# Optimization experiments

Measured on AMD Instinct MI355X. Metric: run time of the kernel, lower is better.

The kernel has to match this reference:

```python
import jax, jax.numpy as jnp
import numpy as np

B, N, M = 2, 8192, 8192


def setup_inputs() -> dict:
    key = jax.random.key(0)
    ks = jax.random.split(key, 12)
    def rn(k, shape):
        return jax.random.normal(k, shape, dtype=jnp.float32)
    return {
        "in_xyz": rn(ks[0], (B, N, 3)),
        "in_rot": rn(ks[1], (B, N, 4)),
        "in_scale": rn(ks[2], (B, N, 3)),
        "in_opacity": rn(ks[3], (B, N, 1)),
        "in_sh_dc": rn(ks[4], (B, N, 3)),
        "in_sh_rest": rn(ks[5], (B, N, 45)),
        "out_xyz": rn(ks[6], (B, M, 3)),
        "out_rot": rn(ks[7], (B, M, 4)),
        "out_scale": rn(ks[8], (B, M, 3)),
        "out_opacity": rn(ks[9], (B, M, 1)),
        "out_sh_dc": rn(ks[10], (B, M, 3)),
        "out_sh_rest": rn(ks[11], (B, M, 45)),
    }


POS_W, ROT_W, SCALE_W, OPAC_W, SH_W = 1.0, 0.5, 0.5, 0.3, 0.2


def _cdist(a, b):
    # a: [B,M,3], b: [B,N,3] -> [B,M,N] Euclidean distance via Gram trick
    sq = (jnp.sum(a * a, -1)[:, :, None] + jnp.sum(b * b, -1)[:, None, :]
          - 2.0 * jnp.einsum('bmd,bnd->bmn', a, b))
    return jnp.sqrt(jnp.maximum(sq, 0.0))


def _gather(x, idx):
    # x: [B,N,D], idx: [B,M] -> [B,M,D]
    return jnp.take_along_axis(x, idx[:, :, None], axis=1)


def reference(in_xyz, in_rot, in_scale, in_opacity, in_sh_dc, in_sh_rest,
              out_xyz, out_rot, out_scale, out_opacity, out_sh_dc, out_sh_rest):
    dist = _cdist(out_xyz, in_xyz)                 # [B,M,N]
    min_out_to_in = jnp.min(dist, axis=2)          # [B,M]
    match_idx = jnp.argmin(dist, axis=2)           # [B,M]
    min_in_to_out = jnp.min(dist, axis=1)          # [B,N]
    pos_loss = (min_out_to_in.mean() + min_in_to_out.mean()) / 2

    matched_rot = _gather(in_rot, match_idx)
    matched_scale = _gather(in_scale, match_idx)
    matched_opacity = _gather(in_opacity, match_idx)
    matched_sh_dc = _gather(in_sh_dc, match_idx)
    matched_sh_rest = _gather(in_sh_rest, match_idx)

    rot_dot = jnp.abs(jnp.sum(out_rot * matched_rot, axis=-1))
    rot_loss = jnp.mean(1.0 - rot_dot)
    scale_loss = jnp.mean(jnp.abs(out_scale - matched_scale))
    opacity_loss = jnp.mean(jnp.abs(out_opacity - matched_opacity))
    sh_loss = (jnp.mean(jnp.abs(out_sh_dc - matched_sh_dc))
               + jnp.mean(jnp.abs(out_sh_rest - matched_sh_rest)))

    total = (POS_W * pos_loss + ROT_W * rot_loss + SCALE_W * scale_loss
             + OPAC_W * opacity_loss + SH_W * sh_loss)
    return total
```

## Files before the change

### kernel.cpp

```cpp
#include <hip/hip_runtime.h>


#define BB 2
#define NN 8192
#define MM 8192
#define TILE_PTS 1024
#define CHUNK_PTS 64
#define CH_STRIDE (CHUNK_PTS * 4 + 4)
#define PM 256
#define NSL 8
#define NPAIR 1024

__device__ __forceinline__ void dmerge(float& d, int& i, float od, int oi) {
    if (od < d || (od == d && oi < i)) { d = od; i = oi; }
}

__device__ __forceinline__ void stage_tile(const float* __restrict__ xyz,
                                           int b, int gtile, int t, float* smem) {
    const uint4* src = (const uint4*)((const char*)xyz +
                       ((size_t)b * NN + (size_t)gtile * TILE_PTS) * 12);
    uint4 wb[3];
#pragma unroll
    for (int k = 0; k < 3; ++k) wb[k] = src[t * 3 + k];
    const unsigned int* w = (const unsigned int*)wb;
    const int p0 = t * 4;
    float4* dst = (float4*)(smem + (p0 >> 6) * CH_STRIDE) + (p0 & 63);
#pragma unroll
    for (int i = 0; i < 4; ++i) {
        float x = __uint_as_float(w[3 * i + 0]);
        float y = __uint_as_float(w[3 * i + 1]);
        float z = __uint_as_float(w[3 * i + 2]);
        float4 v;
        v.x = x; v.y = y; v.z = z;
        v.w = fmaf(z, z, fmaf(y, y, x * x));
        dst[i] = v;
    }
}

__global__ __launch_bounds__(1024) void k_pair(
    const float* __restrict__ in_xyz,
    const float* __restrict__ out_xyz,
    float* __restrict__ outD2,
    int*   __restrict__ outIdx,
    float* __restrict__ inD2) {

    __shared__ float smem[16 * CH_STRIDE];

    const int t  = threadIdx.x;
    const int ml = t >> 4;
    const int c  = t & 15;
    const int blk = blockIdx.x;
    const int side = blk >> 9;
    const int rem = blk & 511;
    const int b  = rem >> 8;
    const int e  = (rem >> 5) & 7;
    const int q0 = (rem & 31) * PM + ml * 4;

    const float* qbase = (side == 0) ? out_xyz : in_xyz;
    const float* pbase = (side == 0) ? in_xyz  : out_xyz;

    float m2x0, m2y0, m2z0, msq0, m2x1, m2y1, m2z1, msq1;
    float m2x2, m2y2, m2z2, msq2, m2x3, m2y3, m2z3, msq3;
#define LOADQ(i)                                                            \
    { const float* qp = qbase + ((size_t)b * MM + q0 + i) * 3;              \
      float ox = qp[0], oy = qp[1], oz = qp[2];                             \
      m2x##i = -2.f * ox; m2y##i = -2.f * oy; m2z##i = -2.f * oz;           \
      msq##i = fmaf(oz, oz, fmaf(oy, oy, ox * ox)); }
    LOADQ(0) LOADQ(1) LOADQ(2) LOADQ(3)
#undef LOADQ

    if (t < 256) stage_tile(pbase, b, e, t, smem);
    __syncthreads();

    const float4* cp = (const float4*)(smem + c * CH_STRIDE);
    const int base = e * TILE_PTS + c * CHUNK_PTS;

    if (side == 0) {
        float bd0 = 3e38f, bd1 = 3e38f, bd2 = 3e38f, bd3 = 3e38f;
        int   bi0 = 0,     bi1 = 0,     bi2 = 0,     bi3 = 0;
#pragma unroll 8
        for (int j = 0; j < CHUNK_PTS; ++j) {
            float4 p = cp[j];
            float k0 = fmaf(p.x, m2x0, fmaf(p.y, m2y0, fmaf(p.z, m2z0, p.w)));
            float k1 = fmaf(p.x, m2x1, fmaf(p.y, m2y1, fmaf(p.z, m2z1, p.w)));
            float k2 = fmaf(p.x, m2x2, fmaf(p.y, m2y2, fmaf(p.z, m2z2, p.w)));
            float k3 = fmaf(p.x, m2x3, fmaf(p.y, m2y3, fmaf(p.z, m2z3, p.w)));
            if (k0 < bd0) { bd0 = k0; bi0 = base + j; }
            if (k1 < bd1) { bd1 = k1; bi1 = base + j; }
            if (k2 < bd2) { bd2 = k2; bi2 = base + j; }
            if (k3 < bd3) { bd3 = k3; bi3 = base + j; }
        }
#pragma unroll
        for (int off = 1; off < 16; off <<= 1) {
            float od; int oi;
            od = __shfl_xor(bd0, off, 64); oi = __shfl_xor(bi0, off, 64); dmerge(bd0, bi0, od, oi);
            od = __shfl_xor(bd1, off, 64); oi = __shfl_xor(bi1, off, 64); dmerge(bd1, bi1, od, oi);
            od = __shfl_xor(bd2, off, 64); oi = __shfl_xor(bi2, off, 64); dmerge(bd2, bi2, od, oi);
            od = __shfl_xor(bd3, off, 64); oi = __shfl_xor(bi3, off, 64); dmerge(bd3, bi3, od, oi);
        }
        if (c == 0) {
            const size_t g = ((size_t)b * MM + q0) * NSL + e;
            outD2[g + 0 * NSL] = bd0 + msq0; outIdx[g + 0 * NSL] = bi0;
            outD2[g + 1 * NSL] = bd1 + msq1; outIdx[g + 1 * NSL] = bi1;
            outD2[g + 2 * NSL] = bd2 + msq2; outIdx[g + 2 * NSL] = bi2;
            outD2[g + 3 * NSL] = bd3 + msq3; outIdx[g + 3 * NSL] = bi3;
        }
    } else {
        float bd0 = 3e38f, bd1 = 3e38f, bd2 = 3e38f, bd3 = 3e38f;
#pragma unroll 8
        for (int j = 0; j < CHUNK_PTS; ++j) {
            float4 p = cp[j];
            float k0 = fmaf(p.x, m2x0, fmaf(p.y, m2y0, fmaf(p.z, m2z0, p.w)));
            float k1 = fmaf(p.x, m2x1, fmaf(p.y, m2y1, fmaf(p.z, m2z1, p.w)));
            float k2 = fmaf(p.x, m2x2, fmaf(p.y, m2y2, fmaf(p.z, m2z2, p.w)));
            float k3 = fmaf(p.x, m2x3, fmaf(p.y, m2y3, fmaf(p.z, m2z3, p.w)));
            bd0 = fminf(bd0, k0);
            bd1 = fminf(bd1, k1);
            bd2 = fminf(bd2, k2);
            bd3 = fminf(bd3, k3);
        }
#pragma unroll
        for (int off = 1; off < 16; off <<= 1) {
            bd0 = fminf(bd0, __shfl_xor(bd0, off, 64));
            bd1 = fminf(bd1, __shfl_xor(bd1, off, 64));
            bd2 = fminf(bd2, __shfl_xor(bd2, off, 64));
            bd3 = fminf(bd3, __shfl_xor(bd3, off, 64));
        }
        if (c == 0) {
            const size_t g = ((size_t)b * NN + q0) * NSL + e;
            inD2[g + 0 * NSL] = bd0 + msq0;
            inD2[g + 1 * NSL] = bd1 + msq1;
            inD2[g + 2 * NSL] = bd2 + msq2;
            inD2[g + 3 * NSL] = bd3 + msq3;
        }
    }
}

__global__ __launch_bounds__(256) void k_epi(
    const float* __restrict__ in_rot,
    const float* __restrict__ in_scale,
    const float* __restrict__ in_op,
    const float* __restrict__ in_dc,
    const float* __restrict__ in_rest,
    const float* __restrict__ out_rot,
    const float* __restrict__ out_scale,
    const float* __restrict__ out_op,
    const float* __restrict__ out_dc,
    const float* __restrict__ out_rest,
    const float* __restrict__ outD2,
    const int*   __restrict__ outIdx,
    const float* __restrict__ inD2,
    float* __restrict__ pout,
    float* __restrict__ pin) {

    const int t = threadIdx.x;
    const int blk = blockIdx.x;

    if (blk < 128) {
        const int u = blk * 256 + t;
        const int m = u >> 1;
        const int h = u & 1;
        const int b = m >> 13;
        float d2 = outD2[(size_t)m * NSL + 0];
        int  idx = outIdx[(size_t)m * NSL + 0];
#pragma unroll
        for (int s = 1; s < NSL; ++s) {
            float ds = outD2[(size_t)m * NSL + s];
            int   is = outIdx[(size_t)m * NSL + s];
            if (ds < d2) { d2 = ds; idx = is; }
        }
        const size_t og = (size_t)m;
        const size_t ig = (size_t)b * NN + (size_t)idx;

        float pos = 0.f, rot = 0.f, scl = 0.f, opa = 0.f, dcv = 0.f, rsv = 0.f;
        if (h == 0) {
            pos = sqrtf(fmaxf(d2, 0.f));
            const float4 orv = ((const float4*)out_rot)[og];
            const float4 irv = ((const float4*)in_rot)[ig];
            float rdot = orv.x * irv.x + orv.y * irv.y + orv.z * irv.z + orv.w * irv.w;
            rot = 1.f - fabsf(rdot);
#pragma unroll
            for (int qq = 0; qq < 3; ++qq) scl += fabsf(out_scale[og * 3 + qq] - in_scale[ig * 3 + qq]);
            opa = fabsf(out_op[og] - in_op[ig]);
#pragma unroll
            for (int qq = 0; qq < 3; ++qq) dcv += fabsf(out_dc[og * 3 + qq] - in_dc[ig * 3 + qq]);
#pragma unroll
            for (int e = 0; e < 22; ++e)
                rsv += fabsf(out_rest[og * 45 + e] - in_rest[ig * 45 + e]);
        } else {
#pragma unroll
            for (int e = 22; e < 45; ++e)
                rsv += fabsf(out_rest[og * 45 + e] - in_rest[ig * 45 + e]);
        }

#pragma unroll
        for (int off = 1; off < 64; off <<= 1) {
            pos += __shfl_xor(pos, off, 64);
            rot += __shfl_xor(rot, off, 64);
            scl += __shfl_xor(scl, off, 64);
            opa += __shfl_xor(opa, off, 64);
            dcv += __shfl_xor(dcv, off, 64);
            rsv += __shfl_xor(rsv, off, 64);
        }
        if ((t & 63) == 0) {
            const size_t w = (size_t)blk * 4 + (t >> 6);
            pout[w * 6 + 0] = pos; pout[w * 6 + 1] = rot; pout[w * 6 + 2] = scl;
            pout[w * 6 + 3] = opa; pout[w * 6 + 4] = dcv; pout[w * 6 + 5] = rsv;
        }
    } else {
        const int g = (blk - 128) * 256 + t;
        float d2 = inD2[(size_t)g * NSL + 0];
#pragma unroll
        for (int s = 1; s < NSL; ++s) d2 = fminf(d2, inD2[(size_t)g * NSL + s]);
        float v = sqrtf(fmaxf(d2, 0.f));
#pragma unroll
        for (int off = 1; off < 64; off <<= 1) v += __shfl_xor(v, off, 64);
        if ((t & 63) == 0) pin[(size_t)(blk - 128) * 4 + (t >> 6)] = v;
    }
}

__global__ __launch_bounds__(256) void k_fin(const float* __restrict__ pout,
                                             const float* __restrict__ pin,
                                             unsigned int* __restrict__ out) {
    __shared__ float red[4][8];
    const int t = threadIdx.x;
    float s0 = 0.f, s1 = 0.f, s2 = 0.f, s3 = 0.f, s4 = 0.f, s5 = 0.f, s6 = 0.f;
    for (int i = t; i < 512; i += 256) {
        s0 += pout[(size_t)i * 6 + 0];
        s1 += pout[(size_t)i * 6 + 1];
        s2 += pout[(size_t)i * 6 + 2];
        s3 += pout[(size_t)i * 6 + 3];
        s4 += pout[(size_t)i * 6 + 4];
        s5 += pout[(size_t)i * 6 + 5];
    }
    if (t < 256) s6 += pin[t];
#pragma unroll
    for (int off = 1; off < 64; off <<= 1) {
        s0 += __shfl_xor(s0, off, 64);
        s1 += __shfl_xor(s1, off, 64);
        s2 += __shfl_xor(s2, off, 64);
        s3 += __shfl_xor(s3, off, 64);
        s4 += __shfl_xor(s4, off, 64);
        s5 += __shfl_xor(s5, off, 64);
        s6 += __shfl_xor(s6, off, 64);
    }
    if ((t & 63) == 0) {
        const int w = t >> 6;
        red[w][0] = s0; red[w][1] = s1; red[w][2] = s2; red[w][3] = s3;
        red[w][4] = s4; red[w][5] = s5; red[w][6] = s6;
    }
    __syncthreads();
    if (t == 0) {
        float a[7];
#pragma unroll
        for (int j = 0; j < 7; ++j)
            a[j] = red[0][j] + red[1][j] + red[2][j] + red[3][j];
        const float inv_bm = 1.0f / (float)(BB * MM);
        const float inv_bn = 1.0f / (float)(BB * NN);
        const float pos = 0.5f * (a[0] * inv_bm + a[6] * inv_bn);
        const float rot = a[1] * inv_bm;
        const float scl = a[2] * inv_bm * (1.f / 3.f);
        const float opa = a[3] * inv_bm;
        const float sh  = a[4] * inv_bm * (1.f / 3.f) + a[5] * inv_bm * (1.f / 45.f);
        const float total = 1.0f * pos + 0.5f * rot + 0.5f * scl + 0.3f * opa + 0.2f * sh;
        unsigned int ub = __float_as_uint(total);
        unsigned int r  = (ub + 0x7FFFu + ((ub >> 16) & 1u)) >> 16;
        if (!(total == total) || fabsf(total) > 1e30f) r = 0x4080u;
        out[0] = (r << 16) | r;
    }
}

extern "C" void kernel_launch(void* const* d_in, const int* in_sizes, int n_in,
                              void* d_out, int out_size, void* d_ws, size_t ws_size,
                              hipStream_t stream) {
    const float* in_xyz    = (const float*)d_in[0];
    const float* in_rot    = (const float*)d_in[1];
    const float* in_scale  = (const float*)d_in[2];
    const float* in_op     = (const float*)d_in[3];
    const float* in_dc     = (const float*)d_in[4];
    const float* in_rest   = (const float*)d_in[5];
    const float* out_xyz   = (const float*)d_in[6];
    const float* out_rot   = (const float*)d_in[7];
    const float* out_scale = (const float*)d_in[8];
    const float* out_op    = (const float*)d_in[9];
    const float* out_dc    = (const float*)d_in[10];
    const float* out_rest  = (const float*)d_in[11];

    float* outD2 = (float*)d_ws;
    int*   outIdx = (int*)(outD2 + (size_t)BB * MM * NSL);
    float* inD2  = (float*)(outIdx + (size_t)BB * MM * NSL);
    float* pout  = inD2 + (size_t)BB * NN * NSL;
    float* pin   = pout + 512 * 6;

    k_pair<<<NPAIR, 1024, 0, stream>>>(in_xyz, out_xyz, outD2, outIdx, inD2);
    k_epi<<<192, 256, 0, stream>>>(in_rot, in_scale, in_op, in_dc, in_rest,
                                   out_rot, out_scale, out_op, out_dc, out_rest,
                                   outD2, outIdx, inD2, pout, pin);
    k_fin<<<1, 256, 0, stream>>>(pout, pin, (unsigned int*)d_out);
}
```

Measured before the change: 115.8 us.

## Compute both directional minima from one distance pass; fuse final reduction into epilogue

The pair kernel now evaluates each query-point distance once. It derives the per-query argmin and, via shuffles plus LDS atomicMin, the per-point column minimum, which removes the separate in-to-out pass and halves the pair blocks. Column partial minima go to a wider 32-slice buffer that the epilogue reduces. The epilogue splits each matched row across 4 threads instead of 2, and the last block, found with an atomic counter, does the final reduction, removing the third kernel launch. In exchange the inner loop gains shuffles and shared atomics, and the epilogue reads a larger partial buffer.

```diff
diff --git a/kernel.cpp b/kernel.cpp
--- a/kernel.cpp
+++ b/kernel.cpp
@@ -7,9 +7,12 @@
 #define TILE_PTS 1024
 #define CHUNK_PTS 64
 #define CH_STRIDE (CHUNK_PTS * 4 + 4)
+#define CM_STRIDE 65
 #define PM 256
 #define NSL 8
-#define NPAIR 1024
+#define GSL 32
+#define NPAIR 512
+#define NEPI 320
 
 __device__ __forceinline__ void dmerge(float& d, int& i, float od, int oi) {
     if (od < d || (od == d && oi < i)) { d = od; i = oi; }
@@ -42,97 +45,83 @@
     const float* __restrict__ out_xyz,
     float* __restrict__ outD2,
     int*   __restrict__ outIdx,
-    float* __restrict__ inD2) {
+    float* __restrict__ inD2s,
+    unsigned int* __restrict__ cnt) {
 
     __shared__ float smem[16 * CH_STRIDE];
+    __shared__ unsigned int cmu[16 * CM_STRIDE];
 
     const int t  = threadIdx.x;
     const int ml = t >> 4;
     const int c  = t & 15;
     const int blk = blockIdx.x;
-    const int side = blk >> 9;
-    const int rem = blk & 511;
-    const int b  = rem >> 8;
-    const int e  = (rem >> 5) & 7;
-    const int q0 = (rem & 31) * PM + ml * 4;
-
-    const float* qbase = (side == 0) ? out_xyz : in_xyz;
-    const float* pbase = (side == 0) ? in_xyz  : out_xyz;
+    const int b  = blk >> 8;
+    const int e  = (blk >> 5) & 7;
+    const int g  = blk & 31;
+    const int q0 = g * PM + ml * 4;
+
+    if (blk == 0 && t == 0) cnt[0] = 0u;
 
     float m2x0, m2y0, m2z0, msq0, m2x1, m2y1, m2z1, msq1;
     float m2x2, m2y2, m2z2, msq2, m2x3, m2y3, m2z3, msq3;
 #define LOADQ(i)                                                            \
-    { const float* qp = qbase + ((size_t)b * MM + q0 + i) * 3;              \
+    { const float* qp = out_xyz + ((size_t)b * MM + q0 + i) * 3;            \
       float ox = qp[0], oy = qp[1], oz = qp[2];                             \
       m2x##i = -2.f * ox; m2y##i = -2.f * oy; m2z##i = -2.f * oz;           \
       msq##i = fmaf(oz, oz, fmaf(oy, oy, ox * ox)); }
     LOADQ(0) LOADQ(1) LOADQ(2) LOADQ(3)
 #undef LOADQ
 
-    if (t < 256) stage_tile(pbase, b, e, t, smem);
+    if (t < 256) stage_tile(in_xyz, b, e, t, smem);
+    for (int i = t; i < 16 * CM_STRIDE; i += 1024) cmu[i] = 0x7F800000u;
     __syncthreads();
 
     const float4* cp = (const float4*)(smem + c * CH_STRIDE);
     const int base = e * TILE_PTS + c * CHUNK_PTS;
-
-    if (side == 0) {
-        float bd0 = 3e38f, bd1 = 3e38f, bd2 = 3e38f, bd3 = 3e38f;
-        int   bi0 = 0,     bi1 = 0,     bi2 = 0,     bi3 = 0;
+    unsigned int* cma = cmu + c * CM_STRIDE;
+    const bool doAtom = ((t & 48) == 0);
+
+    float bd0 = 3e38f, bd1 = 3e38f, bd2 = 3e38f, bd3 = 3e38f;
+    int   bi0 = 0,     bi1 = 0,     bi2 = 0,     bi3 = 0;
 #pragma unroll 8
-        for (int j = 0; j < CHUNK_PTS; ++j) {
-            float4 p = cp[j];
-            float k0 = fmaf(p.x, m2x0, fmaf(p.y, m2y0, fmaf(p.z, m2z0, p.w)));
-            float k1 = fmaf(p.x, m2x1, fmaf(p.y, m2y1, fmaf(p.z, m2z1, p.w)));
-            float k2 = fmaf(p.x, m2x2, fmaf(p.y, m2y2, fmaf(p.z, m2z2, p.w)));
-            float k3 = fmaf(p.x, m2x3, fmaf(p.y, m2y3, fmaf(p.z, m2z3, p.w)));
-            if (k0 < bd0) { bd0 = k0; bi0 = base + j; }
-            if (k1 < bd1) { bd1 = k1; bi1 = base + j; }
-            if (k2 < bd2) { bd2 = k2; bi2 = base + j; }
-            if (k3 < bd3) { bd3 = k3; bi3 = base + j; }
-        }
-#pragma unroll
-        for (int off = 1; off < 16; off <<= 1) {
-            float od; int oi;
-            od = __shfl_xor(bd0, off, 64); oi = __shfl_xor(bi0, off, 64); dmerge(bd0, bi0, od, oi);
-            od = __shfl_xor(bd1, off, 64); oi = __shfl_xor(bi1, off, 64); dmerge(bd1, bi1, od, oi);
-            od = __shfl_xor(bd2, off, 64); oi = __shfl_xor(bi2, off, 64); dmerge(bd2, bi2, od, oi);
-            od = __shfl_xor(bd3, off, 64); oi = __shfl_xor(bi3, off, 64); dmerge(bd3, bi3, od, oi);
-        }
-        if (c == 0) {
-            const size_t g = ((size_t)b * MM + q0) * NSL + e;
-            outD2[g + 0 * NSL] = bd0 + msq0; outIdx[g + 0 * NSL] = bi0;
-            outD2[g + 1 * NSL] = bd1 + msq1; outIdx[g + 1 * NSL] = bi1;
-            outD2[g + 2 * NSL] = bd2 + msq2; outIdx[g + 2 * NSL] = bi2;
-            outD2[g + 3 * NSL] = bd3 + msq3; outIdx[g + 3 * NSL] = bi3;
-        }
-    } else {
-        float bd0 = 3e38f, bd1 = 3e38f, bd2 = 3e38f, bd3 = 3e38f;
-#pragma unroll 8
-        for (int j = 0; j < CHUNK_PTS; ++j) {
-            float4 p = cp[j];
-            float k0 = fmaf(p.x, m2x0, fmaf(p.y, m2y0, fmaf(p.z, m2z0, p.w)));
-            float k1 = fmaf(p.x, m2x1, fmaf(p.y, m2y1, fmaf(p.z, m2z1, p.w)));
-            float k2 = fmaf(p.x, m2x2, fmaf(p.y, m2y2, fmaf(p.z, m2z2, p.w)));
-            float k3 = fmaf(p.x, m2x3, fmaf(p.y, m2y3, fmaf(p.z, m2z3, p.w)));
-            bd0 = fminf(bd0, k0);
-            bd1 = fminf(bd1, k1);
-            bd2 = fminf(bd2, k2);
-            bd3 = fminf(bd3, k3);
-        }
-#pragma unroll
-        for (int off = 1; off < 16; off <<= 1) {
-            bd0 = fminf(bd0, __shfl_xor(bd0, off, 64));
-            bd1 = fminf(bd1, __shfl_xor(bd1, off, 64));
-            bd2 = fminf(bd2, __shfl_xor(bd2, off, 64));
-            bd3 = fminf(bd3, __shfl_xor(bd3, off, 64));
-        }
-        if (c == 0) {
-            const size_t g = ((size_t)b * NN + q0) * NSL + e;
-            inD2[g + 0 * NSL] = bd0 + msq0;
-            inD2[g + 1 * NSL] = bd1 + msq1;
-            inD2[g + 2 * NSL] = bd2 + msq2;
-            inD2[g + 3 * NSL] = bd3 + msq3;
-        }
+    for (int j = 0; j < CHUNK_PTS; ++j) {
+        float4 p = cp[j];
+        float w0 = p.w + msq0, w1 = p.w + msq1, w2 = p.w + msq2, w3 = p.w + msq3;
+        float k0 = fmaf(p.x, m2x0, fmaf(p.y, m2y0, fmaf(p.z, m2z0, w0)));
+        float k1 = fmaf(p.x, m2x1, fmaf(p.y, m2y1, fmaf(p.z, m2z1, w1)));
+        float k2 = fmaf(p.x, m2x2, fmaf(p.y, m2y2, fmaf(p.z, m2z2, w2)));
+        float k3 = fmaf(p.x, m2x3, fmaf(p.y, m2y3, fmaf(p.z, m2z3, w3)));
+        if (k0 < bd0) { bd0 = k0; bi0 = base + j; }
+        if (k1 < bd1) { bd1 = k1; bi1 = base + j; }
+        if (k2 < bd2) { bd2 = k2; bi2 = base + j; }
+        if (k3 < bd3) { bd3 = k3; bi3 = base + j; }
+        float mm = fminf(fminf(k0, k1), fminf(k2, k3));
+        mm = fmaxf(mm, 0.0f);
+        mm = fminf(mm, __shfl_xor(mm, 16, 64));
+        mm = fminf(mm, __shfl_xor(mm, 32, 64));
+        if (doAtom) atomicMin(cma + j, __float_as_uint(mm));
+    }
+
+#pragma unroll
+    for (int off = 1; off < 16; off <<= 1) {
+        float od; int oi;
+        od = __shfl_xor(bd0, off, 64); oi = __shfl_xor(bi0, off, 64); dmerge(bd0, bi0, od, oi);
+        od = __shfl_xor(bd1, off, 64); oi = __shfl_xor(bi1, off, 64); dmerge(bd1, bi1, od, oi);
+        od = __shfl_xor(bd2, off, 64); oi = __shfl_xor(bi2, off, 64); dmerge(bd2, bi2, od, oi);
+        od = __shfl_xor(bd3, off, 64); oi = __shfl_xor(bi3, off, 64); dmerge(bd3, bi3, od, oi);
+    }
+    if (c == 0) {
+        const size_t gi = ((size_t)b * MM + q0) * NSL + e;
+        outD2[gi + 0 * NSL] = bd0; outIdx[gi + 0 * NSL] = bi0;
+        outD2[gi + 1 * NSL] = bd1; outIdx[gi + 1 * NSL] = bi1;
+        outD2[gi + 2 * NSL] = bd2; outIdx[gi + 2 * NSL] = bi2;
+        outD2[gi + 3 * NSL] = bd3; outIdx[gi + 3 * NSL] = bi3;
+    }
+
+    __syncthreads();
+    {
+        float v = __uint_as_float(cmu[(t >> 6) * CM_STRIDE + (t & 63)]);
+        inD2s[(size_t)g * (BB * NN) + (size_t)b * NN + e * TILE_PTS + t] = v;
     }
 }
 
@@ -149,25 +138,30 @@
     const float* __restrict__ out_rest,
     const float* __restrict__ outD2,
     const int*   __restrict__ outIdx,
-    const float* __restrict__ inD2,
+    const float* __restrict__ inD2s,
     float* __restrict__ pout,
-    float* __restrict__ pin) {
-
+    float* __restrict__ pin,
+    unsigned int* __restrict__ cnt,
+    unsigned int* __restrict__ outw) {
+
+    __shared__ float red[4][8];
+    __shared__ int lastFlag;
     const int t = threadIdx.x;
     const int blk = blockIdx.x;
 
-    if (blk < 128) {
+    if (blk < 256) {
         const int u = blk * 256 + t;
-        const int m = u >> 1;
-        const int h = u & 1;
+        const int m = u >> 2;
+        const int h = u & 3;
         const int b = m >> 13;
-        float d2 = outD2[(size_t)m * NSL + 0];
-        int  idx = outIdx[(size_t)m * NSL + 0];
-#pragma unroll
-        for (int s = 1; s < NSL; ++s) {
-            float ds = outD2[(size_t)m * NSL + s];
-            int   is = outIdx[(size_t)m * NSL + s];
-            if (ds < d2) { d2 = ds; idx = is; }
+        float2 dv = ((const float2*)outD2)[(size_t)m * 4 + h];
+        int2   iv = ((const int2*)outIdx)[(size_t)m * 4 + h];
+        float d2 = dv.x; int idx = iv.x;
+        if (dv.y < d2) { d2 = dv.y; idx = iv.y; }
+        {
+            float od; int oi;
+            od = __shfl_xor(d2, 1, 64); oi = __shfl_xor(idx, 1, 64); dmerge(d2, idx, od, oi);
+            od = __shfl_xor(d2, 2, 64); oi = __shfl_xor(idx, 2, 64); dmerge(d2, idx, od, oi);
         }
         const size_t og = (size_t)m;
         const size_t ig = (size_t)b * NN + (size_t)idx;
@@ -179,11 +173,13 @@
             const float4 irv = ((const float4*)in_rot)[ig];
             float rdot = orv.x * irv.x + orv.y * irv.y + orv.z * irv.z + orv.w * irv.w;
             rot = 1.f - fabsf(rdot);
-#pragma unroll
-            for (int qq = 0; qq < 3; ++qq) scl += fabsf(out_scale[og * 3 + qq] - in_scale[ig * 3 + qq]);
+        } else if (h == 1) {
+#pragma unroll
+            for (int q = 0; q < 3; ++q) scl += fabsf(out_scale[og * 3 + q] - in_scale[ig * 3 + q]);
             opa = fabsf(out_op[og] - in_op[ig]);
 #pragma unroll
-            for (int qq = 0; qq < 3; ++qq) dcv += fabsf(out_dc[og * 3 + qq] - in_dc[ig * 3 + qq]);
+            for (int q = 0; q < 3; ++q) dcv += fabsf(out_dc[og * 3 + q] - in_dc[ig * 3 + q]);
+        } else if (h == 2) {
 #pragma unroll
             for (int e = 0; e < 22; ++e)
                 rsv += fabsf(out_rest[og * 45 + e] - in_rest[ig * 45 + e]);
@@ -208,24 +204,29 @@
             pout[w * 6 + 3] = opa; pout[w * 6 + 4] = dcv; pout[w * 6 + 5] = rsv;
         }
     } else {
-        const int g = (blk - 128) * 256 + t;
-        float d2 = inD2[(size_t)g * NSL + 0];
-#pragma unroll
-        for (int s = 1; s < NSL; ++s) d2 = fminf(d2, inD2[(size_t)g * NSL + s]);
+        const int n = (blk - 256) * 256 + t;
+        float d2 = inD2s[n];
+#pragma unroll
+        for (int s = 1; s < GSL; ++s)
+            d2 = fminf(d2, inD2s[(size_t)s * (BB * NN) + n]);
         float v = sqrtf(fmaxf(d2, 0.f));
 #pragma unroll
         for (int off = 1; off < 64; off <<= 1) v += __shfl_xor(v, off, 64);
-        if ((t & 63) == 0) pin[(size_t)(blk - 128) * 4 + (t >> 6)] = v;
-    }
-}
-
-__global__ __launch_bounds__(256) void k_fin(const float* __restrict__ pout,
-                                             const float* __restrict__ pin,
-                                             unsigned int* __restrict__ out) {
-    __shared__ float red[4][8];
-    const int t = threadIdx.x;
+        if ((t & 63) == 0) pin[(size_t)(blk - 256) * 4 + (t >> 6)] = v;
+    }
+
+    __syncthreads();
+    if (t == 0) {
+        __threadfence();
+        unsigned int old = atomicAdd(cnt, 1u);
+        lastFlag = (old == (unsigned)(NEPI - 1));
+    }
+    __syncthreads();
+    if (!lastFlag) return;
+    __threadfence();
+
     float s0 = 0.f, s1 = 0.f, s2 = 0.f, s3 = 0.f, s4 = 0.f, s5 = 0.f, s6 = 0.f;
-    for (int i = t; i < 512; i += 256) {
+    for (int i = t; i < 1024; i += 256) {
         s0 += pout[(size_t)i * 6 + 0];
         s1 += pout[(size_t)i * 6 + 1];
         s2 += pout[(size_t)i * 6 + 2];
@@ -233,7 +234,7 @@
         s4 += pout[(size_t)i * 6 + 4];
         s5 += pout[(size_t)i * 6 + 5];
     }
-    if (t < 256) s6 += pin[t];
+    s6 = pin[t];
 #pragma unroll
     for (int off = 1; off < 64; off <<= 1) {
         s0 += __shfl_xor(s0, off, 64);
@@ -266,7 +267,7 @@
         unsigned int ub = __float_as_uint(total);
         unsigned int r  = (ub + 0x7FFFu + ((ub >> 16) & 1u)) >> 16;
         if (!(total == total) || fabsf(total) > 1e30f) r = 0x4080u;
-        out[0] = (r << 16) | r;
+        outw[0] = (r << 16) | r;
     }
 }
 
@@ -288,13 +289,14 @@
 
     float* outD2 = (float*)d_ws;
     int*   outIdx = (int*)(outD2 + (size_t)BB * MM * NSL);
-    float* inD2  = (float*)(outIdx + (size_t)BB * MM * NSL);
-    float* pout  = inD2 + (size_t)BB * NN * NSL;
-    float* pin   = pout + 512 * 6;
-
-    k_pair<<<NPAIR, 1024, 0, stream>>>(in_xyz, out_xyz, outD2, outIdx, inD2);
-    k_epi<<<192, 256, 0, stream>>>(in_rot, in_scale, in_op, in_dc, in_rest,
-                                   out_rot, out_scale, out_op, out_dc, out_rest,
-                                   outD2, outIdx, inD2, pout, pin);
-    k_fin<<<1, 256, 0, stream>>>(pout, pin, (unsigned int*)d_out);
-}
+    float* inD2s = (float*)(outIdx + (size_t)BB * MM * NSL);
+    float* pout  = inD2s + (size_t)GSL * BB * NN;
+    float* pin   = pout + 1024 * 6;
+    unsigned int* cnt = (unsigned int*)(pin + 256);
+
+    k_pair<<<NPAIR, 1024, 0, stream>>>(in_xyz, out_xyz, outD2, outIdx, inD2s, cnt);
+    k_epi<<<NEPI, 256, 0, stream>>>(in_rot, in_scale, in_op, in_dc, in_rest,
+                                    out_rot, out_scale, out_op, out_dc, out_rest,
+                                    outD2, outIdx, inD2s, pout, pin, cnt,
+                                    (unsigned int*)d_out);
+}
```

Result: slower. 135.2 us (+16.8%).

## Fuse final reduction into epilogue via atomic last-block and widen epilogue parallelism

Applied to the files above, without the earlier changes.

Removes the separate single-block finalize kernel by having the last epilogue block, detected with an atomic counter reset in the pair kernel, perform the final reduction. The epilogue now uses four threads per output point instead of two: each thread takes two slices, a shuffle merges the argmin, and the attribute loads are split across four roles. The in-side reduction switches to float4 vector loads. This saves one kernel launch and raises parallelism in the gather phase, at the cost of an atomic, fences and a serialized tail block.

```diff
diff --git a/kernel.cpp b/kernel.cpp
--- a/kernel.cpp
+++ b/kernel.cpp
@@ -10,6 +10,7 @@
 #define PM 256
 #define NSL 8
 #define NPAIR 1024
+#define NEPI 320
 
 __device__ __forceinline__ void dmerge(float& d, int& i, float od, int oi) {
     if (od < d || (od == d && oi < i)) { d = od; i = oi; }
@@ -42,7 +43,8 @@
     const float* __restrict__ out_xyz,
     float* __restrict__ outD2,
     int*   __restrict__ outIdx,
-    float* __restrict__ inD2) {
+    float* __restrict__ inD2,
+    unsigned int* __restrict__ cnt) {
 
     __shared__ float smem[16 * CH_STRIDE];
 
@@ -55,6 +57,8 @@
     const int b  = rem >> 8;
     const int e  = (rem >> 5) & 7;
     const int q0 = (rem & 31) * PM + ml * 4;
+
+    if (blk == 0 && t == 0) cnt[0] = 0u;
 
     const float* qbase = (side == 0) ? out_xyz : in_xyz;
     const float* pbase = (side == 0) ? in_xyz  : out_xyz;
@@ -151,23 +155,28 @@
     const int*   __restrict__ outIdx,
     const float* __restrict__ inD2,
     float* __restrict__ pout,
-    float* __restrict__ pin) {
-
+    float* __restrict__ pin,
+    unsigned int* __restrict__ cnt,
+    unsigned int* __restrict__ outw) {
+
+    __shared__ float red[4][8];
+    __shared__ int lastFlag;
     const int t = threadIdx.x;
     const int blk = blockIdx.x;
 
-    if (blk < 128) {
+    if (blk < 256) {
         const int u = blk * 256 + t;
-        const int m = u >> 1;
-        const int h = u & 1;
+        const int m = u >> 2;
+        const int h = u & 3;
         const int b = m >> 13;
-        float d2 = outD2[(size_t)m * NSL + 0];
-        int  idx = outIdx[(size_t)m * NSL + 0];
-#pragma unroll
-        for (int s = 1; s < NSL; ++s) {
-            float ds = outD2[(size_t)m * NSL + s];
-            int   is = outIdx[(size_t)m * NSL + s];
-            if (ds < d2) { d2 = ds; idx = is; }
+        float2 dv = ((const float2*)outD2)[(size_t)m * 4 + h];
+        int2   iv = ((const int2*)outIdx)[(size_t)m * 4 + h];
+        float d2 = dv.x; int idx = iv.x;
+        if (dv.y < d2) { d2 = dv.y; idx = iv.y; }
+        {
+            float od; int oi;
+            od = __shfl_xor(d2, 1, 64); oi = __shfl_xor(idx, 1, 64); dmerge(d2, idx, od, oi);
+            od = __shfl_xor(d2, 2, 64); oi = __shfl_xor(idx, 2, 64); dmerge(d2, idx, od, oi);
         }
         const size_t og = (size_t)m;
         const size_t ig = (size_t)b * NN + (size_t)idx;
@@ -179,11 +188,13 @@
             const float4 irv = ((const float4*)in_rot)[ig];
             float rdot = orv.x * irv.x + orv.y * irv.y + orv.z * irv.z + orv.w * irv.w;
             rot = 1.f - fabsf(rdot);
-#pragma unroll
-            for (int qq = 0; qq < 3; ++qq) scl += fabsf(out_scale[og * 3 + qq] - in_scale[ig * 3 + qq]);
+        } else if (h == 1) {
+#pragma unroll
+            for (int q = 0; q < 3; ++q) scl += fabsf(out_scale[og * 3 + q] - in_scale[ig * 3 + q]);
             opa = fabsf(out_op[og] - in_op[ig]);
 #pragma unroll
-            for (int qq = 0; qq < 3; ++qq) dcv += fabsf(out_dc[og * 3 + qq] - in_dc[ig * 3 + qq]);
+            for (int q = 0; q < 3; ++q) dcv += fabsf(out_dc[og * 3 + q] - in_dc[ig * 3 + q]);
+        } else if (h == 2) {
 #pragma unroll
             for (int e = 0; e < 22; ++e)
                 rsv += fabsf(out_rest[og * 45 + e] - in_rest[ig * 45 + e]);
@@ -208,24 +219,29 @@
             pout[w * 6 + 3] = opa; pout[w * 6 + 4] = dcv; pout[w * 6 + 5] = rsv;
         }
     } else {
-        const int g = (blk - 128) * 256 + t;
-        float d2 = inD2[(size_t)g * NSL + 0];
-#pragma unroll
-        for (int s = 1; s < NSL; ++s) d2 = fminf(d2, inD2[(size_t)g * NSL + s]);
+        const int n = (blk - 256) * 256 + t;
+        const float4 a = ((const float4*)inD2)[(size_t)n * 2 + 0];
+        const float4 c4 = ((const float4*)inD2)[(size_t)n * 2 + 1];
+        float d2 = fminf(fminf(fminf(a.x, a.y), fminf(a.z, a.w)),
+                         fminf(fminf(c4.x, c4.y), fminf(c4.z, c4.w)));
         float v = sqrtf(fmaxf(d2, 0.f));
 #pragma unroll
         for (int off = 1; off < 64; off <<= 1) v += __shfl_xor(v, off, 64);
-        if ((t & 63) == 0) pin[(size_t)(blk - 128) * 4 + (t >> 6)] = v;
-    }
-}
-
-__global__ __launch_bounds__(256) void k_fin(const float* __restrict__ pout,
-                                             const float* __restrict__ pin,
-                                             unsigned int* __restrict__ out) {
-    __shared__ float red[4][8];
-    const int t = threadIdx.x;
+        if ((t & 63) == 0) pin[(size_t)(blk - 256) * 4 + (t >> 6)] = v;
+    }
+
+    __syncthreads();
+    if (t == 0) {
+        __threadfence();
+        unsigned int old = atomicAdd(cnt, 1u);
+        lastFlag = (old == (unsigned)(NEPI - 1));
+    }
+    __syncthreads();
+    if (!lastFlag) return;
+    __threadfence();
+
     float s0 = 0.f, s1 = 0.f, s2 = 0.f, s3 = 0.f, s4 = 0.f, s5 = 0.f, s6 = 0.f;
-    for (int i = t; i < 512; i += 256) {
+    for (int i = t; i < 1024; i += 256) {
         s0 += pout[(size_t)i * 6 + 0];
         s1 += pout[(size_t)i * 6 + 1];
         s2 += pout[(size_t)i * 6 + 2];
@@ -233,7 +249,7 @@
         s4 += pout[(size_t)i * 6 + 4];
         s5 += pout[(size_t)i * 6 + 5];
     }
-    if (t < 256) s6 += pin[t];
+    s6 = pin[t];
 #pragma unroll
     for (int off = 1; off < 64; off <<= 1) {
         s0 += __shfl_xor(s0, off, 64);
@@ -266,7 +282,7 @@
         unsigned int ub = __float_as_uint(total);
         unsigned int r  = (ub + 0x7FFFu + ((ub >> 16) & 1u)) >> 16;
         if (!(total == total) || fabsf(total) > 1e30f) r = 0x4080u;
-        out[0] = (r << 16) | r;
+        outw[0] = (r << 16) | r;
     }
 }
 
@@ -290,11 +306,12 @@
     int*   outIdx = (int*)(outD2 + (size_t)BB * MM * NSL);
     float* inD2  = (float*)(outIdx + (size_t)BB * MM * NSL);
     float* pout  = inD2 + (size_t)BB * NN * NSL;
-    float* pin   = pout + 512 * 6;
-
-    k_pair<<<NPAIR, 1024, 0, stream>>>(in_xyz, out_xyz, outD2, outIdx, inD2);
-    k_epi<<<192, 256, 0, stream>>>(in_rot, in_scale, in_op, in_dc, in_rest,
-                                   out_rot, out_scale, out_op, out_dc, out_rest,
-                                   outD2, outIdx, inD2, pout, pin);
-    k_fin<<<1, 256, 0, stream>>>(pout, pin, (unsigned int*)d_out);
-}
+    float* pin   = pout + 1024 * 6;
+    unsigned int* cnt = (unsigned int*)(pin + 256);
+
+    k_pair<<<NPAIR, 1024, 0, stream>>>(in_xyz, out_xyz, outD2, outIdx, inD2, cnt);
+    k_epi<<<NEPI, 256, 0, stream>>>(in_rot, in_scale, in_op, in_dc, in_rest,
+                                    out_rot, out_scale, out_op, out_dc, out_rest,
+                                    outD2, outIdx, inD2, pout, pin, cnt,
+                                    (unsigned int*)d_out);
+}
```

New measurement: 122.9 us. 6.1% more time.

## Use packed FP32 FMA over an SoA pair layout in the pairwise distance kernel

Applied to the files above, without the earlier changes.

Stages reference points in LDS as interleaved pairs (x0,x1,y0,y1 / z0,z1,w0,w1) so each thread evaluates two candidate points at once with v_pk_fma_f32 inline asm. This halves the FMA instruction count in the inner distance loop. Blocks shrink to 512 threads with 128 queries each and the grid doubles, and launch bounds request 4 blocks per CU. In exchange the per-lane argmin tracking is duplicated, which needs extra registers and compares, and an extra merge is needed before the shuffle reduction.

```diff
diff --git a/kernel.cpp b/kernel.cpp
--- a/kernel.cpp
+++ b/kernel.cpp
@@ -4,134 +4,157 @@
 #define BB 2
 #define NN 8192
 #define MM 8192
-#define TILE_PTS 1024
-#define CHUNK_PTS 64
-#define CH_STRIDE (CHUNK_PTS * 4 + 4)
-#define PM 256
+#define PB 1024
+#define QB 128
 #define NSL 8
-#define NPAIR 1024
+#define NPAIR 2048
+
+typedef float vf2 __attribute__((ext_vector_type(2)));
+
+__device__ __forceinline__ vf2 pk_fma(vf2 a, vf2 b, vf2 c) {
+    vf2 d;
+    asm("v_pk_fma_f32 %0, %1, %2, %3" : "=v"(d) : "v"(a), "v"(b), "v"(c));
+    return d;
+}
 
 __device__ __forceinline__ void dmerge(float& d, int& i, float od, int oi) {
     if (od < d || (od == d && oi < i)) { d = od; i = oi; }
 }
 
-__device__ __forceinline__ void stage_tile(const float* __restrict__ xyz,
-                                           int b, int gtile, int t, float* smem) {
-    const uint4* src = (const uint4*)((const char*)xyz +
-                       ((size_t)b * NN + (size_t)gtile * TILE_PTS) * 12);
-    uint4 wb[3];
-#pragma unroll
-    for (int k = 0; k < 3; ++k) wb[k] = src[t * 3 + k];
-    const unsigned int* w = (const unsigned int*)wb;
-    const int p0 = t * 4;
-    float4* dst = (float4*)(smem + (p0 >> 6) * CH_STRIDE) + (p0 & 63);
-#pragma unroll
-    for (int i = 0; i < 4; ++i) {
-        float x = __uint_as_float(w[3 * i + 0]);
-        float y = __uint_as_float(w[3 * i + 1]);
-        float z = __uint_as_float(w[3 * i + 2]);
-        float4 v;
-        v.x = x; v.y = y; v.z = z;
-        v.w = fmaf(z, z, fmaf(y, y, x * x));
-        dst[i] = v;
-    }
-}
-
-__global__ __launch_bounds__(1024) void k_pair(
+__global__ __launch_bounds__(512, 4) void k_pair(
     const float* __restrict__ in_xyz,
     const float* __restrict__ out_xyz,
     float* __restrict__ outD2,
     int*   __restrict__ outIdx,
     float* __restrict__ inD2) {
 
-    __shared__ float smem[16 * CH_STRIDE];
+    __shared__ float4 xy[16 * 33];
+    __shared__ float4 zw[16 * 33];
 
     const int t  = threadIdx.x;
     const int ml = t >> 4;
     const int c  = t & 15;
     const int blk = blockIdx.x;
-    const int side = blk >> 9;
-    const int rem = blk & 511;
-    const int b  = rem >> 8;
-    const int e  = (rem >> 5) & 7;
-    const int q0 = (rem & 31) * PM + ml * 4;
+    const int side = blk >> 10;
+    const int rem = blk & 1023;
+    const int b  = rem >> 9;
+    const int e  = (rem >> 6) & 7;
+    const int q0 = (rem & 63) * QB + ml * 4;
 
     const float* qbase = (side == 0) ? out_xyz : in_xyz;
     const float* pbase = (side == 0) ? in_xyz  : out_xyz;
 
-    float m2x0, m2y0, m2z0, msq0, m2x1, m2y1, m2z1, msq1;
-    float m2x2, m2y2, m2z2, msq2, m2x3, m2y3, m2z3, msq3;
+    vf2 X0, Y0, Z0, X1, Y1, Z1, X2, Y2, Z2, X3, Y3, Z3;
+    float msq0, msq1, msq2, msq3;
 #define LOADQ(i)                                                            \
     { const float* qp = qbase + ((size_t)b * MM + q0 + i) * 3;              \
       float ox = qp[0], oy = qp[1], oz = qp[2];                             \
-      m2x##i = -2.f * ox; m2y##i = -2.f * oy; m2z##i = -2.f * oz;           \
+      float mx = -2.f * ox, my = -2.f * oy, mz = -2.f * oz;                 \
+      X##i = (vf2){mx, mx}; Y##i = (vf2){my, my}; Z##i = (vf2){mz, mz};     \
       msq##i = fmaf(oz, oz, fmaf(oy, oy, ox * ox)); }
     LOADQ(0) LOADQ(1) LOADQ(2) LOADQ(3)
 #undef LOADQ
 
-    if (t < 256) stage_tile(pbase, b, e, t, smem);
+    if (t < 256) {
+        const uint4* src = (const uint4*)((const char*)pbase +
+                           ((size_t)b * NN + (size_t)e * PB) * 12);
+        uint4 wb[3];
+#pragma unroll
+        for (int k = 0; k < 3; ++k) wb[k] = src[t * 3 + k];
+        const float* w = (const float*)wb;
+        const int ch = t >> 4;
+        const int u0 = (2 * t) & 31;
+        float x0 = w[0], y0 = w[1],  z0 = w[2];
+        float x1 = w[3], y1 = w[4],  z1 = w[5];
+        float x2 = w[6], y2 = w[7],  z2 = w[8];
+        float x3 = w[9], y3 = w[10], z3 = w[11];
+        float w0 = fmaf(z0, z0, fmaf(y0, y0, x0 * x0));
+        float w1 = fmaf(z1, z1, fmaf(y1, y1, x1 * x1));
+        float w2 = fmaf(z2, z2, fmaf(y2, y2, x2 * x2));
+        float w3 = fmaf(z3, z3, fmaf(y3, y3, x3 * x3));
+        xy[ch * 33 + u0]     = make_float4(x0, x1, y0, y1);
+        zw[ch * 33 + u0]     = make_float4(z0, z1, w0, w1);
+        xy[ch * 33 + u0 + 1] = make_float4(x2, x3, y2, y3);
+        zw[ch * 33 + u0 + 1] = make_float4(z2, z3, w2, w3);
+    }
     __syncthreads();
 
-    const float4* cp = (const float4*)(smem + c * CH_STRIDE);
-    const int base = e * TILE_PTS + c * CHUNK_PTS;
+    const int c33 = c * 33;
+    const int base = e * PB + c * 64;
 
     if (side == 0) {
-        float bd0 = 3e38f, bd1 = 3e38f, bd2 = 3e38f, bd3 = 3e38f;
-        int   bi0 = 0,     bi1 = 0,     bi2 = 0,     bi3 = 0;
+        vf2 bd0 = {3e38f, 3e38f}, bd1 = bd0, bd2 = bd0, bd3 = bd0;
+        int bix0 = 0, biy0 = 0, bix1 = 0, biy1 = 0;
+        int bix2 = 0, biy2 = 0, bix3 = 0, biy3 = 0;
 #pragma unroll 8
-        for (int j = 0; j < CHUNK_PTS; ++j) {
-            float4 p = cp[j];
-            float k0 = fmaf(p.x, m2x0, fmaf(p.y, m2y0, fmaf(p.z, m2z0, p.w)));
-            float k1 = fmaf(p.x, m2x1, fmaf(p.y, m2y1, fmaf(p.z, m2z1, p.w)));
-            float k2 = fmaf(p.x, m2x2, fmaf(p.y, m2y2, fmaf(p.z, m2z2, p.w)));
-            float k3 = fmaf(p.x, m2x3, fmaf(p.y, m2y3, fmaf(p.z, m2z3, p.w)));
-            if (k0 < bd0) { bd0 = k0; bi0 = base + j; }
-            if (k1 < bd1) { bd1 = k1; bi1 = base + j; }
-            if (k2 < bd2) { bd2 = k2; bi2 = base + j; }
-            if (k3 < bd3) { bd3 = k3; bi3 = base + j; }
-        }
+        for (int u = 0; u < 32; ++u) {
+            const float4 a = xy[c33 + u];
+            const float4 s = zw[c33 + u];
+            const vf2 xp = {a.x, a.y}, yp = {a.z, a.w};
+            const vf2 zp = {s.x, s.y}, wp = {s.z, s.w};
+            const int j0 = base + 2 * u;
+#define STEP(i)                                                             \
+            { vf2 kp = pk_fma(xp, X##i, pk_fma(yp, Y##i,                    \
+                              pk_fma(zp, Z##i, wp)));                       \
+              if (kp.x < bd##i.x) { bd##i.x = kp.x; bix##i = j0; }          \
+              if (kp.y < bd##i.y) { bd##i.y = kp.y; biy##i = j0 + 1; } }
+            STEP(0) STEP(1) STEP(2) STEP(3)
+#undef STEP
+        }
+        float d0 = bd0.x, d1 = bd1.x, d2 = bd2.x, d3 = bd3.x;
+        int   i0 = bix0,  i1 = bix1,  i2 = bix2,  i3 = bix3;
+        dmerge(d0, i0, bd0.y, biy0);
+        dmerge(d1, i1, bd1.y, biy1);
+        dmerge(d2, i2, bd2.y, biy2);
+        dmerge(d3, i3, bd3.y, biy3);
 #pragma unroll
         for (int off = 1; off < 16; off <<= 1) {
             float od; int oi;
-            od = __shfl_xor(bd0, off, 64); oi = __shfl_xor(bi0, off, 64); dmerge(bd0, bi0, od, oi);
-            od = __shfl_xor(bd1, off, 64); oi = __shfl_xor(bi1, off, 64); dmerge(bd1, bi1, od, oi);
-            od = __shfl_xor(bd2, off, 64); oi = __shfl_xor(bi2, off, 64); dmerge(bd2, bi2, od, oi);
-            od = __shfl_xor(bd3, off, 64); oi = __shfl_xor(bi3, off, 64); dmerge(bd3, bi3, od, oi);
+            od = __shfl_xor(d0, off, 64); oi = __shfl_xor(i0, off, 64); dmerge(d0, i0, od, oi);
+            od = __shfl_xor(d1, off, 64); oi = __shfl_xor(i1, off, 64); dmerge(d1, i1, od, oi);
+            od = __shfl_xor(d2, off, 64); oi = __shfl_xor(i2, off, 64); dmerge(d2, i2, od, oi);
+            od = __shfl_xor(d3, off, 64); oi = __shfl_xor(i3, off, 64); dmerge(d3, i3, od, oi);
         }
         if (c == 0) {
-            const size_t g = ((size_t)b * MM + q0) * NSL + e;
-            outD2[g + 0 * NSL] = bd0 + msq0; outIdx[g + 0 * NSL] = bi0;
-            outD2[g + 1 * NSL] = bd1 + msq1; outIdx[g + 1 * NSL] = bi1;
-            outD2[g + 2 * NSL] = bd2 + msq2; outIdx[g + 2 * NSL] = bi2;
-            outD2[g + 3 * NSL] = bd3 + msq3; outIdx[g + 3 * NSL] = bi3;
+            const size_t gi = ((size_t)b * MM + q0) * NSL + e;
+            outD2[gi + 0 * NSL] = d0 + msq0; outIdx[gi + 0 * NSL] = i0;
+            outD2[gi + 1 * NSL] = d1 + msq1; outIdx[gi + 1 * NSL] = i1;
+            outD2[gi + 2 * NSL] = d2 + msq2; outIdx[gi + 2 * NSL] = i2;
+            outD2[gi + 3 * NSL] = d3 + msq3; outIdx[gi + 3 * NSL] = i3;
         }
     } else {
-        float bd0 = 3e38f, bd1 = 3e38f, bd2 = 3e38f, bd3 = 3e38f;
+        vf2 bd0 = {3e38f, 3e38f}, bd1 = bd0, bd2 = bd0, bd3 = bd0;
 #pragma unroll 8
-        for (int j = 0; j < CHUNK_PTS; ++j) {
-            float4 p = cp[j];
-            float k0 = fmaf(p.x, m2x0, fmaf(p.y, m2y0, fmaf(p.z, m2z0, p.w)));
-            float k1 = fmaf(p.x, m2x1, fmaf(p.y, m2y1, fmaf(p.z, m2z1, p.w)));
-            float k2 = fmaf(p.x, m2x2, fmaf(p.y, m2y2, fmaf(p.z, m2z2, p.w)));
-            float k3 = fmaf(p.x, m2x3, fmaf(p.y, m2y3, fmaf(p.z, m2z3, p.w)));
-            bd0 = fminf(bd0, k0);
-            bd1 = fminf(bd1, k1);
-            bd2 = fminf(bd2, k2);
-            bd3 = fminf(bd3, k3);
-        }
+        for (int u = 0; u < 32; ++u) {
+            const float4 a = xy[c33 + u];
+            const float4 s = zw[c33 + u];
+            const vf2 xp = {a.x, a.y}, yp = {a.z, a.w};
+            const vf2 zp = {s.x, s.y}, wp = {s.z, s.w};
+#define STEP(i)                                                             \
+            { vf2 kp = pk_fma(xp, X##i, pk_fma(yp, Y##i,                    \
+                              pk_fma(zp, Z##i, wp)));                       \
+              bd##i.x = fminf(bd##i.x, kp.x);                               \
+              bd##i.y = fminf(bd##i.y, kp.y); }
+            STEP(0) STEP(1) STEP(2) STEP(3)
+#undef STEP
+        }
+        float d0 = fminf(bd0.x, bd0.y);
+        float d1 = fminf(bd1.x, bd1.y);
+        float d2 = fminf(bd2.x, bd2.y);
+        float d3 = fminf(bd3.x, bd3.y);
 #pragma unroll
         for (int off = 1; off < 16; off <<= 1) {
-            bd0 = fminf(bd0, __shfl_xor(bd0, off, 64));
-            bd1 = fminf(bd1, __shfl_xor(bd1, off, 64));
-            bd2 = fminf(bd2, __shfl_xor(bd2, off, 64));
-            bd3 = fminf(bd3, __shfl_xor(bd3, off, 64));
+            d0 = fminf(d0, __shfl_xor(d0, off, 64));
+            d1 = fminf(d1, __shfl_xor(d1, off, 64));
+            d2 = fminf(d2, __shfl_xor(d2, off, 64));
+            d3 = fminf(d3, __shfl_xor(d3, off, 64));
         }
         if (c == 0) {
-            const size_t g = ((size_t)b * NN + q0) * NSL + e;
-            inD2[g + 0 * NSL] = bd0 + msq0;
-            inD2[g + 1 * NSL] = bd1 + msq1;
-            inD2[g + 2 * NSL] = bd2 + msq2;
-            inD2[g + 3 * NSL] = bd3 + msq3;
+            const size_t gi = ((size_t)b * NN + q0) * NSL + e;
+            inD2[gi + 0 * NSL] = d0 + msq0;
+            inD2[gi + 1 * NSL] = d1 + msq1;
+            inD2[gi + 2 * NSL] = d2 + msq2;
+            inD2[gi + 3 * NSL] = d3 + msq3;
         }
     }
 }
@@ -292,7 +315,7 @@
     float* pout  = inD2 + (size_t)BB * NN * NSL;
     float* pin   = pout + 512 * 6;
 
-    k_pair<<<NPAIR, 1024, 0, stream>>>(in_xyz, out_xyz, outD2, outIdx, inD2);
+    k_pair<<<NPAIR, 512, 0, stream>>>(in_xyz, out_xyz, outD2, outIdx, inD2);
     k_epi<<<192, 256, 0, stream>>>(in_rot, in_scale, in_op, in_dc, in_rest,
                                    out_rot, out_scale, out_op, out_dc, out_rest,
                                    outD2, outIdx, inD2, pout, pin);
```

Result: slower. 118.6 us (+2.4%).
